# Kernel tuning notes

Measured on AMD Instinct MI355X. Metric: run time of the kernel, lower is better.

## Reference

```python
import jax, jax.numpy as jnp
import numpy as np

N_EMBD = 2048
N_HEAD = 16
D_HEAD = N_EMBD // N_HEAD


def setup_inputs() -> dict:
    key = jax.random.key(0)
    k1, k2, k3 = jax.random.split(key, 3)
    x = jax.random.normal(k1, (2, 2048, N_EMBD), dtype=jnp.float32)
    # torch Linear stores weight as [out, in]; kept in that layout
    w_qkv = jax.random.normal(k2, (3 * N_EMBD, N_EMBD), dtype=jnp.float32) * (1.0 / np.sqrt(N_EMBD))
    w_out = jax.random.normal(k3, (N_EMBD, N_EMBD), dtype=jnp.float32) * (1.0 / np.sqrt(N_EMBD))
    return {"x": x, "w_qkv": w_qkv, "w_out": w_out}


def reference(x, w_qkv, w_out):
    B, T, C = x.shape
    H, D = N_HEAD, D_HEAD
    qkv = jnp.einsum('btc,oc->bto', x, w_qkv)            # [B,T,3C]
    qkv = qkv.reshape(B, T, 3, H, D)
    q = jnp.transpose(qkv[:, :, 0], (0, 2, 1, 3))        # [B,H,T,D]
    k = jnp.transpose(qkv[:, :, 1], (0, 2, 1, 3))
    v = jnp.transpose(qkv[:, :, 2], (0, 2, 1, 3))
    scale = 1.0 / np.sqrt(D).astype(np.float32)
    att = jnp.einsum('bhqd,bhkd->bhqk', q, k) * scale    # [B,H,T,T]
    causal = jnp.tril(jnp.ones((T, T), dtype=bool))
    att = jnp.where(causal[None, None], att, jnp.finfo(att.dtype).min)
    att = jax.nn.softmax(att, axis=-1)
    y = jnp.einsum('bhqk,bhkd->bhqd', att, v)            # [B,H,T,D]
    y = jnp.transpose(y, (0, 2, 1, 3)).reshape(B, T, C)
    return jnp.einsum('btc,oc->bto', y, w_out)
```

## Files before the change

### kernel.cpp

```cpp
#include <hip/hip_runtime.h>
#include <stdint.h>


typedef __attribute__((ext_vector_type(8))) short bf16x8;
typedef __attribute__((ext_vector_type(8))) unsigned short u16x8;
typedef __attribute__((ext_vector_type(4))) unsigned short u16x4;
typedef __attribute__((ext_vector_type(4))) float f32x4;

#define MFMA16(a, b, c) __builtin_amdgcn_mfma_f32_16x16x32_bf16((a), (b), (c), 0, 0, 0)

__device__ __forceinline__ unsigned short f2bf(float f) {
  union { float f; uint32_t u; } v; v.f = f;
  uint32_t r = v.u + 0x7FFFu + ((v.u >> 16) & 1u);
  return (unsigned short)(r >> 16);
}

__device__ __forceinline__ void gld_lds16(const unsigned short* g, unsigned short* lds) {
  __builtin_amdgcn_global_load_lds(
      (const __attribute__((address_space(1))) void*)g,
      (__attribute__((address_space(3))) void*)lds, 16, 0, 0);
}

__global__ __launch_bounds__(256) void cvt_bf16(const float* __restrict__ in,
                                                unsigned short* __restrict__ out, int n8) {
  int stride = gridDim.x * blockDim.x;
  for (int i = blockIdx.x * blockDim.x + threadIdx.x; i < n8; i += stride) {
    float4 a = reinterpret_cast<const float4*>(in)[i * 2];
    float4 b = reinterpret_cast<const float4*>(in)[i * 2 + 1];
    u16x8 o;
    o[0] = f2bf(a.x); o[1] = f2bf(a.y); o[2] = f2bf(a.z); o[3] = f2bf(a.w);
    o[4] = f2bf(b.x); o[5] = f2bf(b.y); o[6] = f2bf(b.z); o[7] = f2bf(b.w);
    reinterpret_cast<u16x8*>(out)[i] = o;
  }
}

__device__ __forceinline__ void gemm128_core(const unsigned short* __restrict__ A,
                                             const unsigned short* __restrict__ Bt,
                                             int K, int brow, int bcol,
                                             unsigned short* lds_a, unsigned short* lds_b,
                                             f32x4 acc[4][4]) {
  const int tid = threadIdx.x;
  const int l   = tid & 63;
  const int w   = tid >> 6;
  const int wr  = (w >> 1) << 6;
  const int wc  = (w & 1) << 6;

  const int srow = tid >> 2;
  const int sswz = (tid & 3) ^ ((srow >> 1) & 3);
  const unsigned short* gA0 = A  + (size_t)(brow + srow) * K + 8 * sswz;
  const unsigned short* gA1 = gA0 + (size_t)64 * K;
  const unsigned short* gB0 = Bt + (size_t)(bcol + srow) * K + 8 * sswz;
  const unsigned short* gB1 = gB0 + (size_t)64 * K;

  unsigned short* la0 = lds_a + tid * 8;
  unsigned short* la1 = lds_a + (256 + tid) * 8;
  unsigned short* lb0 = lds_b + tid * 8;
  unsigned short* lb1 = lds_b + (256 + tid) * 8;

  const int fm    = l & 15;
  const int fswz8 = 8 * ((l >> 4) ^ ((fm >> 1) & 3));

  for (int k0 = 0; k0 < K; k0 += 32) {
    gld_lds16(gA0, la0);
    gld_lds16(gA1, la1);
    gld_lds16(gB0, lb0);
    gld_lds16(gB1, lb1);
    gA0 += 32; gA1 += 32; gB0 += 32; gB1 += 32;
    __syncthreads();
    bf16x8 af[4], bfv[4];
#pragma unroll
    for (int i = 0; i < 4; i++)
      af[i] = *(const bf16x8*)&lds_a[(wr + i * 16 + fm) * 32 + fswz8];
#pragma unroll
    for (int j = 0; j < 4; j++)
      bfv[j] = *(const bf16x8*)&lds_b[(wc + j * 16 + fm) * 32 + fswz8];
#pragma unroll
    for (int i = 0; i < 4; i++)
#pragma unroll
      for (int j = 0; j < 4; j++)
        acc[i][j] = MFMA16(af[i], bfv[j], acc[i][j]);
    __syncthreads();
  }
}

__global__ __launch_bounds__(256) void gemm_qkv(const unsigned short* __restrict__ xb,
                                                const unsigned short* __restrict__ wqb,
                                                unsigned short* __restrict__ Qb,
                                                unsigned short* __restrict__ Kb,
                                                unsigned short* __restrict__ Vtb) {
  __shared__ alignas(16) unsigned short lds_a[128 * 32];
  __shared__ alignas(16) unsigned short lds_b[128 * 32];
  f32x4 acc[4][4];
#pragma unroll
  for (int i = 0; i < 4; i++)
#pragma unroll
    for (int j = 0; j < 4; j++) acc[i][j] = (f32x4){0.f, 0.f, 0.f, 0.f};

  const int brow = blockIdx.y << 7;
  const int bcol = blockIdx.x << 7;
  gemm128_core(xb, wqb, 2048, brow, bcol, lds_a, lds_b, acc);

  const int l = threadIdx.x & 63;
  const int w = threadIdx.x >> 6;
  const int wr = (w >> 1) << 6, wc = (w & 1) << 6;
  const int which = bcol >> 11;
  const int bh = ((brow >> 11) << 4) | ((bcol >> 7) & 15);
  const int tbase = (brow & 2047) + wr + ((l >> 4) << 2);

#pragma unroll
  for (int i = 0; i < 4; i++) {
    const int t0 = tbase + i * 16;
#pragma unroll
    for (int j = 0; j < 4; j++) {
      const int d = wc + j * 16 + (l & 15);
      if (which == 2) {
        u16x4 pk;
#pragma unroll
        for (int r = 0; r < 4; r++) pk[r] = f2bf(acc[i][j][r]);
        *reinterpret_cast<u16x4*>(&Vtb[((size_t)bh * 128 + d) * 2048 + t0]) = pk;
      } else {
        unsigned short* dst = (which == 0 ? Qb : Kb) + ((size_t)bh * 2048 + t0) * 128 + d;
#pragma unroll
        for (int r = 0; r < 4; r++) dst[(size_t)r * 128] = f2bf(acc[i][j][r]);
      }
    }
  }
}

__global__ __launch_bounds__(256) void gemm_out(const unsigned short* __restrict__ yb,
                                                const unsigned short* __restrict__ wob,
                                                float* __restrict__ out) {
  __shared__ alignas(16) unsigned short lds_a[128 * 32];
  __shared__ alignas(16) unsigned short lds_b[128 * 32];
  f32x4 acc[4][4];
#pragma unroll
  for (int i = 0; i < 4; i++)
#pragma unroll
    for (int j = 0; j < 4; j++) acc[i][j] = (f32x4){0.f, 0.f, 0.f, 0.f};

  const int brow = blockIdx.y << 7;
  const int bcol = blockIdx.x << 7;
  gemm128_core(yb, wob, 2048, brow, bcol, lds_a, lds_b, acc);

  const int l = threadIdx.x & 63;
  const int w = threadIdx.x >> 6;
  const int wr = (w >> 1) << 6, wc = (w & 1) << 6;
#pragma unroll
  for (int i = 0; i < 4; i++) {
    const int m0 = brow + wr + i * 16 + ((l >> 4) << 2);
#pragma unroll
    for (int j = 0; j < 4; j++) {
      const int n = bcol + wc + j * 16 + (l & 15);
#pragma unroll
      for (int r = 0; r < 4; r++) out[(size_t)(m0 + r) * 2048 + n] = acc[i][j][r];
    }
  }
}

__device__ __forceinline__ void stage_kv64(const unsigned short* __restrict__ Kg,
                                           const unsigned short* __restrict__ Vg,
                                           int kv0, unsigned short* dk,
                                           unsigned short* dv, int tid) {
#pragma unroll
  for (int c = 0; c < 4; c++) {
    int s = c * 256 + tid;
    int row = s >> 4, g = s & 15;
    gld_lds16(&Kg[(size_t)(kv0 + row) * 128 + 8 * (g ^ (row & 7))], &dk[s * 8]);
  }
#pragma unroll
  for (int c = 0; c < 4; c++) {
    int s = c * 256 + tid;
    int row = s >> 3, g = s & 7;
    gld_lds16(&Vg[(size_t)row * 2048 + kv0 + 8 * (g ^ (row & 7))], &dv[s * 8]);
  }
}

__device__ __forceinline__ void attn_tile_step(const bf16x8 qf[4], f32x4 yacc[8],
                                               float mrow[4], float lrow[4],
                                               int qw0, int kv0,
                                               const unsigned short* kb,
                                               const unsigned short* vb,
                                               unsigned short* pw, int l) {
  const float SC = 0.12752585f;
  f32x4 sfr[4];
  __builtin_amdgcn_s_setprio(1);
#pragma unroll
  for (int kt = 0; kt < 4; kt++) {
    const int kr = kt * 16 + (l & 15);
    f32x4 s4 = (f32x4){0.f, 0.f, 0.f, 0.f};
#pragma unroll
    for (int ds = 0; ds < 4; ds++) {
      bf16x8 kfr = *(const bf16x8*)&kb[kr * 128 + 8 * (((ds << 2) + (l >> 4)) ^ (kr & 7))];
      s4 = MFMA16(qf[ds], kfr, s4);
    }
    sfr[kt] = s4;
  }
  __builtin_amdgcn_s_setprio(0);
  const bool need_mask = (kv0 + 63 > qw0);
#pragma unroll
  for (int kt = 0; kt < 4; kt++)
#pragma unroll
    for (int r = 0; r < 4; r++) {
      float sv = sfr[kt][r] * SC;
      if (need_mask) {
        int qa = qw0 + ((l >> 4) << 2) + r;
        int ka = kv0 + kt * 16 + (l & 15);
        sv = (ka > qa) ? -1e30f : sv;
      }
      sfr[kt][r] = sv;
    }
  float rmax[4];
#pragma unroll
  for (int r = 0; r < 4; r++) {
    float m = fmaxf(fmaxf(sfr[0][r], sfr[1][r]), fmaxf(sfr[2][r], sfr[3][r]));
    m = fmaxf(m, __shfl_xor(m, 1));
    m = fmaxf(m, __shfl_xor(m, 2));
    m = fmaxf(m, __shfl_xor(m, 4));
    m = fmaxf(m, __shfl_xor(m, 8));
    rmax[r] = m;
  }
  bool sm = (rmax[0] <= mrow[0] + 8.f) && (rmax[1] <= mrow[1] + 8.f) &&
            (rmax[2] <= mrow[2] + 8.f) && (rmax[3] <= mrow[3] + 8.f);
  if (!__all(sm)) {
    float f[4];
#pragma unroll
    for (int r = 0; r < 4; r++) {
      float mn = fmaxf(mrow[r], rmax[r]);
      f[r] = exp2f(mrow[r] - mn);
      mrow[r] = mn;
      lrow[r] *= f[r];
    }
#pragma unroll
    for (int dt = 0; dt < 8; dt++)
#pragma unroll
      for (int r = 0; r < 4; r++) yacc[dt][r] *= f[r];
  }
  float rsum[4] = {0.f, 0.f, 0.f, 0.f};
#pragma unroll
  for (int kt = 0; kt < 4; kt++)
#pragma unroll
    for (int r = 0; r < 4; r++) {
      float p = exp2f(sfr[kt][r] - mrow[r]);
      rsum[r] += p;
      int row = ((l >> 4) << 2) + r;
      int k = kt * 16 + (l & 15);
      pw[row * 64 + (((k >> 3) ^ (row & 7)) << 3) + (k & 7)] = f2bf(p);
    }
#pragma unroll
  for (int r = 0; r < 4; r++) {
    float s = rsum[r];
    s += __shfl_xor(s, 1);
    s += __shfl_xor(s, 2);
    s += __shfl_xor(s, 4);
    s += __shfl_xor(s, 8);
    lrow[r] += s;
  }
  asm volatile("s_waitcnt lgkmcnt(0)" ::: "memory");
  __builtin_amdgcn_sched_barrier(0);
  __builtin_amdgcn_s_setprio(1);
#pragma unroll
  for (int ks = 0; ks < 2; ks++) {
    const int prow = l & 15;
    bf16x8 pa = *(const bf16x8*)&pw[prow * 64 + ((((ks << 2) + (l >> 4)) ^ (prow & 7)) << 3)];
#pragma unroll
    for (int dt = 0; dt < 8; dt++) {
      const int d = dt * 16 + (l & 15);
      bf16x8 vv = *(const bf16x8*)&vb[d * 64 + ((((ks << 2) + (l >> 4)) ^ (d & 7)) << 3)];
      yacc[dt] = MFMA16(pa, vv, yacc[dt]);
    }
  }
  __builtin_amdgcn_s_setprio(0);
  asm volatile("s_waitcnt lgkmcnt(0)" ::: "memory");
}

__global__ __launch_bounds__(256, 2) void attn_kernel(const unsigned short* __restrict__ Qb,
                                                      const unsigned short* __restrict__ Kb,
                                                      const unsigned short* __restrict__ Vtb,
                                                      unsigned short* __restrict__ Yb) {
  __shared__ alignas(16) unsigned short lds_k[2][64 * 128];
  __shared__ alignas(16) unsigned short lds_v[2][128 * 64];
  __shared__ alignas(16) unsigned short p_lds[4][16 * 64];

  const int tid = threadIdx.x;
  const int l = tid & 63;
  const int w = tid >> 6;

  const int bid = blockIdx.x;
  const int xcd = bid & 7;
  const int loc = bid >> 3;
  const int bh = xcd * 4 + (loc >> 4);
  const int jidx = loc & 15;

  const int b = bh >> 4, h = bh & 15;

  const unsigned short* Qg = Qb + (size_t)bh * 2048 * 128;
  const unsigned short* Kg = Kb + (size_t)bh * 2048 * 128;
  const unsigned short* Vg = Vtb + (size_t)bh * 128 * 2048;

  const int j_lo = jidx, j_hi = 31 - jidx;
  const int qw0_lo = (j_lo << 6) + (w << 4);
  const int qw0_hi = (j_hi << 6) + (w << 4);

  bf16x8 qf_lo[4], qf_hi[4];
#pragma unroll
  for (int ds = 0; ds < 4; ds++) {
    qf_lo[ds] = *(const bf16x8*)&Qg[(size_t)(qw0_lo + (l & 15)) * 128 + ds * 32 + 8 * (l >> 4)];
    qf_hi[ds] = *(const bf16x8*)&Qg[(size_t)(qw0_hi + (l & 15)) * 128 + ds * 32 + 8 * (l >> 4)];
  }

  f32x4 yacc_lo[8], yacc_hi[8];
#pragma unroll
  for (int dt = 0; dt < 8; dt++) {
    yacc_lo[dt] = (f32x4){0.f, 0.f, 0.f, 0.f};
    yacc_hi[dt] = (f32x4){0.f, 0.f, 0.f, 0.f};
  }
  float mrow_lo[4], lrow_lo[4], mrow_hi[4], lrow_hi[4];
#pragma unroll
  for (int r = 0; r < 4; r++) {
    mrow_lo[r] = -1e30f; lrow_lo[r] = 0.f;
    mrow_hi[r] = -1e30f; lrow_hi[r] = 0.f;
  }

  const int nkv = j_hi + 1;

  stage_kv64(Kg, Vg, 0, lds_k[0], lds_v[0], tid);
  asm volatile("s_waitcnt vmcnt(0)" ::: "memory");
  __syncthreads();

  for (int t = 0; t < nkv; t++) {
    const int kv0 = t << 6;
    const int buf = t & 1;
    const unsigned short* kb = lds_k[buf];
    const unsigned short* vb = lds_v[buf];
    if (t + 1 < nkv)
      stage_kv64(Kg, Vg, kv0 + 64, lds_k[buf ^ 1], lds_v[buf ^ 1], tid);

    if (kv0 <= qw0_lo + 15)
      attn_tile_step(qf_lo, yacc_lo, mrow_lo, lrow_lo, qw0_lo, kv0, kb, vb, p_lds[w], l);
    attn_tile_step(qf_hi, yacc_hi, mrow_hi, lrow_hi, qw0_hi, kv0, kb, vb, p_lds[w], l);

    asm volatile("s_waitcnt vmcnt(0)" ::: "memory");
    __syncthreads();
  }

#pragma unroll
  for (int dt = 0; dt < 8; dt++)
#pragma unroll
    for (int r = 0; r < 4; r++) {
      int qa_lo = qw0_lo + ((l >> 4) << 2) + r;
      int qa_hi = qw0_hi + ((l >> 4) << 2) + r;
      Yb[((size_t)(b * 2048 + qa_lo)) * 2048 + h * 128 + dt * 16 + (l & 15)] =
          f2bf(yacc_lo[dt][r] / lrow_lo[r]);
      Yb[((size_t)(b * 2048 + qa_hi)) * 2048 + h * 128 + dt * 16 + (l & 15)] =
          f2bf(yacc_hi[dt][r] / lrow_hi[r]);
    }
}

extern "C" void kernel_launch(void* const* d_in, const int* in_sizes, int n_in,
                              void* d_out, int out_size, void* d_ws, size_t ws_size,
                              hipStream_t stream) {
  const float* x    = (const float*)d_in[0];
  const float* wqkv = (const float*)d_in[1];
  const float* wout = (const float*)d_in[2];
  float* out = (float*)d_out;

  unsigned short* ws  = (unsigned short*)d_ws;
  unsigned short* xb  = ws;
  unsigned short* wqb = xb + (size_t)8388608;
  unsigned short* wob = wqb + (size_t)12582912;
  unsigned short* Qb  = wob + (size_t)4194304;
  unsigned short* Kb  = Qb + (size_t)8388608;
  unsigned short* Vtb = Kb + (size_t)8388608;
  unsigned short* Yb  = Vtb + (size_t)8388608;

  cvt_bf16<<<1024, 256, 0, stream>>>(x, xb, 8388608 / 8);
  cvt_bf16<<<1024, 256, 0, stream>>>(wqkv, wqb, 12582912 / 8);
  cvt_bf16<<<512, 256, 0, stream>>>(wout, wob, 4194304 / 8);
  gemm_qkv<<<dim3(48, 32), 256, 0, stream>>>(xb, wqb, Qb, Kb, Vtb);
  attn_kernel<<<512, 256, 0, stream>>>(Qb, Kb, Vtb, Yb);
  gemm_out<<<dim3(16, 32), 256, 0, stream>>>(Yb, wob, out);
}
```

Measured before the change: 284.3 us.

## Fuse bf16 conversions, defer softmax row-sum reductions, and split P buffers

The three fp32-to-bf16 conversion launches become one grid-stride kernel, removing two launches. In attention, the row-max shuffle reduction now runs only when the lane-local max exceeds the threshold. The row-sum shuffle reduction is deferred to the end as per-lane partial sums. The lo and hi tiles get separate P LDS buffers, which lets the trailing lgkmcnt wait be dropped. This adds 8 KB of LDS per block, which may affect occupancy at two blocks per CU.

```diff
diff --git a/kernel.cpp b/kernel.cpp
--- a/kernel.cpp
+++ b/kernel.cpp
@@ -21,17 +21,27 @@
       (__attribute__((address_space(3))) void*)lds, 16, 0, 0);
 }
 
-__global__ __launch_bounds__(256) void cvt_bf16(const float* __restrict__ in,
-                                                unsigned short* __restrict__ out, int n8) {
-  int stride = gridDim.x * blockDim.x;
-  for (int i = blockIdx.x * blockDim.x + threadIdx.x; i < n8; i += stride) {
-    float4 a = reinterpret_cast<const float4*>(in)[i * 2];
-    float4 b = reinterpret_cast<const float4*>(in)[i * 2 + 1];
-    u16x8 o;
-    o[0] = f2bf(a.x); o[1] = f2bf(a.y); o[2] = f2bf(a.z); o[3] = f2bf(a.w);
-    o[4] = f2bf(b.x); o[5] = f2bf(b.y); o[6] = f2bf(b.z); o[7] = f2bf(b.w);
-    reinterpret_cast<u16x8*>(out)[i] = o;
-  }
+__device__ __forceinline__ void cvt8(const float* __restrict__ in,
+                                     unsigned short* __restrict__ out, int i) {
+  float4 a = reinterpret_cast<const float4*>(in)[i * 2];
+  float4 b = reinterpret_cast<const float4*>(in)[i * 2 + 1];
+  u16x8 o;
+  o[0] = f2bf(a.x); o[1] = f2bf(a.y); o[2] = f2bf(a.z); o[3] = f2bf(a.w);
+  o[4] = f2bf(b.x); o[5] = f2bf(b.y); o[6] = f2bf(b.z); o[7] = f2bf(b.w);
+  reinterpret_cast<u16x8*>(out)[i] = o;
+}
+
+__global__ __launch_bounds__(256) void cvt_all(const float* __restrict__ x,
+                                               const float* __restrict__ wq,
+                                               const float* __restrict__ wo,
+                                               unsigned short* __restrict__ xb,
+                                               unsigned short* __restrict__ wqb,
+                                               unsigned short* __restrict__ wob) {
+  const int stride = gridDim.x * blockDim.x;
+  const int t0 = blockIdx.x * blockDim.x + threadIdx.x;
+  for (int i = t0; i < 1048576; i += stride) cvt8(x, xb, i);
+  for (int i = t0; i < 1572864; i += stride) cvt8(wq, wqb, i);
+  for (int i = t0; i < 524288; i += stride) cvt8(wo, wob, i);
 }
 
 __device__ __forceinline__ void gemm128_core(const unsigned short* __restrict__ A,
@@ -176,7 +186,7 @@
 }
 
 __device__ __forceinline__ void attn_tile_step(const bf16x8 qf[4], f32x4 yacc[8],
-                                               float mrow[4], float lrow[4],
+                                               float mrow[4], float lsum[4],
                                                int qw0, int kv0,
                                                const unsigned short* kb,
                                                const unsigned short* vb,
@@ -209,52 +219,41 @@
       }
       sfr[kt][r] = sv;
     }
-  float rmax[4];
-#pragma unroll
-  for (int r = 0; r < 4; r++) {
-    float m = fmaxf(fmaxf(sfr[0][r], sfr[1][r]), fmaxf(sfr[2][r], sfr[3][r]));
-    m = fmaxf(m, __shfl_xor(m, 1));
-    m = fmaxf(m, __shfl_xor(m, 2));
-    m = fmaxf(m, __shfl_xor(m, 4));
-    m = fmaxf(m, __shfl_xor(m, 8));
-    rmax[r] = m;
-  }
-  bool sm = (rmax[0] <= mrow[0] + 8.f) && (rmax[1] <= mrow[1] + 8.f) &&
-            (rmax[2] <= mrow[2] + 8.f) && (rmax[3] <= mrow[3] + 8.f);
+  float prmax[4];
+#pragma unroll
+  for (int r = 0; r < 4; r++)
+    prmax[r] = fmaxf(fmaxf(sfr[0][r], sfr[1][r]), fmaxf(sfr[2][r], sfr[3][r]));
+  bool sm = (prmax[0] <= mrow[0] + 8.f) && (prmax[1] <= mrow[1] + 8.f) &&
+            (prmax[2] <= mrow[2] + 8.f) && (prmax[3] <= mrow[3] + 8.f);
   if (!__all(sm)) {
     float f[4];
 #pragma unroll
     for (int r = 0; r < 4; r++) {
-      float mn = fmaxf(mrow[r], rmax[r]);
+      float m = prmax[r];
+      m = fmaxf(m, __shfl_xor(m, 1));
+      m = fmaxf(m, __shfl_xor(m, 2));
+      m = fmaxf(m, __shfl_xor(m, 4));
+      m = fmaxf(m, __shfl_xor(m, 8));
+      float mn = fmaxf(mrow[r], m);
       f[r] = exp2f(mrow[r] - mn);
       mrow[r] = mn;
-      lrow[r] *= f[r];
+      lsum[r] *= f[r];
     }
 #pragma unroll
     for (int dt = 0; dt < 8; dt++)
 #pragma unroll
       for (int r = 0; r < 4; r++) yacc[dt][r] *= f[r];
   }
-  float rsum[4] = {0.f, 0.f, 0.f, 0.f};
 #pragma unroll
   for (int kt = 0; kt < 4; kt++)
 #pragma unroll
     for (int r = 0; r < 4; r++) {
       float p = exp2f(sfr[kt][r] - mrow[r]);
-      rsum[r] += p;
+      lsum[r] += p;
       int row = ((l >> 4) << 2) + r;
       int k = kt * 16 + (l & 15);
       pw[row * 64 + (((k >> 3) ^ (row & 7)) << 3) + (k & 7)] = f2bf(p);
     }
-#pragma unroll
-  for (int r = 0; r < 4; r++) {
-    float s = rsum[r];
-    s += __shfl_xor(s, 1);
-    s += __shfl_xor(s, 2);
-    s += __shfl_xor(s, 4);
-    s += __shfl_xor(s, 8);
-    lrow[r] += s;
-  }
   asm volatile("s_waitcnt lgkmcnt(0)" ::: "memory");
   __builtin_amdgcn_sched_barrier(0);
   __builtin_amdgcn_s_setprio(1);
@@ -270,7 +269,6 @@
     }
   }
   __builtin_amdgcn_s_setprio(0);
-  asm volatile("s_waitcnt lgkmcnt(0)" ::: "memory");
 }
 
 __global__ __launch_bounds__(256, 2) void attn_kernel(const unsigned short* __restrict__ Qb,
@@ -279,7 +277,7 @@
                                                       unsigned short* __restrict__ Yb) {
   __shared__ alignas(16) unsigned short lds_k[2][64 * 128];
   __shared__ alignas(16) unsigned short lds_v[2][128 * 64];
-  __shared__ alignas(16) unsigned short p_lds[4][16 * 64];
+  __shared__ alignas(16) unsigned short p_lds[8][16 * 64];
 
   const int tid = threadIdx.x;
   const int l = tid & 63;
@@ -314,11 +312,11 @@
     yacc_lo[dt] = (f32x4){0.f, 0.f, 0.f, 0.f};
     yacc_hi[dt] = (f32x4){0.f, 0.f, 0.f, 0.f};
   }
-  float mrow_lo[4], lrow_lo[4], mrow_hi[4], lrow_hi[4];
+  float mrow_lo[4], lsum_lo[4], mrow_hi[4], lsum_hi[4];
 #pragma unroll
   for (int r = 0; r < 4; r++) {
-    mrow_lo[r] = -1e30f; lrow_lo[r] = 0.f;
-    mrow_hi[r] = -1e30f; lrow_hi[r] = 0.f;
+    mrow_lo[r] = -1e30f; lsum_lo[r] = 0.f;
+    mrow_hi[r] = -1e30f; lsum_hi[r] = 0.f;
   }
 
   const int nkv = j_hi + 1;
@@ -336,13 +334,25 @@
       stage_kv64(Kg, Vg, kv0 + 64, lds_k[buf ^ 1], lds_v[buf ^ 1], tid);
 
     if (kv0 <= qw0_lo + 15)
-      attn_tile_step(qf_lo, yacc_lo, mrow_lo, lrow_lo, qw0_lo, kv0, kb, vb, p_lds[w], l);
-    attn_tile_step(qf_hi, yacc_hi, mrow_hi, lrow_hi, qw0_hi, kv0, kb, vb, p_lds[w], l);
+      attn_tile_step(qf_lo, yacc_lo, mrow_lo, lsum_lo, qw0_lo, kv0, kb, vb, p_lds[w], l);
+    attn_tile_step(qf_hi, yacc_hi, mrow_hi, lsum_hi, qw0_hi, kv0, kb, vb, p_lds[4 + w], l);
 
     asm volatile("s_waitcnt vmcnt(0)" ::: "memory");
     __syncthreads();
   }
 
+  float lrow_lo[4], lrow_hi[4];
+#pragma unroll
+  for (int r = 0; r < 4; r++) {
+    float s = lsum_lo[r];
+    s += __shfl_xor(s, 1); s += __shfl_xor(s, 2);
+    s += __shfl_xor(s, 4); s += __shfl_xor(s, 8);
+    lrow_lo[r] = s;
+    float u = lsum_hi[r];
+    u += __shfl_xor(u, 1); u += __shfl_xor(u, 2);
+    u += __shfl_xor(u, 4); u += __shfl_xor(u, 8);
+    lrow_hi[r] = u;
+  }
 #pragma unroll
   for (int dt = 0; dt < 8; dt++)
 #pragma unroll
@@ -373,9 +383,7 @@
   unsigned short* Vtb = Kb + (size_t)8388608;
   unsigned short* Yb  = Vtb + (size_t)8388608;
 
-  cvt_bf16<<<1024, 256, 0, stream>>>(x, xb, 8388608 / 8);
-  cvt_bf16<<<1024, 256, 0, stream>>>(wqkv, wqb, 12582912 / 8);
-  cvt_bf16<<<512, 256, 0, stream>>>(wout, wob, 4194304 / 8);
+  cvt_all<<<2048, 256, 0, stream>>>(x, wqkv, wout, xb, wqb, wob);
   gemm_qkv<<<dim3(48, 32), 256, 0, stream>>>(xb, wqb, Qb, Kb, Vtb);
   attn_kernel<<<512, 256, 0, stream>>>(Qb, Kb, Vtb, Yb);
   gemm_out<<<dim3(16, 32), 256, 0, stream>>>(Yb, wob, out);
```

Result: faster. 263.9 us (-7.2%).
